# Kernel optimization log

Measured on AMD Instinct MI355X. Metric: run time of the kernel, lower is better.

## Reference

```python
import jax, jax.numpy as jnp
import numpy as np

DIM = 1024
N_HEADS = 16
HEAD_DIM = DIM // N_HEADS


def setup_inputs() -> dict:
    key = jax.random.key(0)
    ks = jax.random.split(key, 5)
    x = jax.random.normal(ks[0], (2, 2048, DIM), dtype=jnp.float32)
    # nn.Linear-style init scale
    s = 1.0 / np.sqrt(DIM)
    W_qkv = jax.random.uniform(ks[1], (DIM, 3 * DIM), jnp.float32, -s, s)
    b_qkv = jax.random.uniform(ks[2], (3 * DIM,), jnp.float32, -s, s)
    W_proj = jax.random.uniform(ks[3], (DIM, DIM), jnp.float32, -s, s)
    b_proj = jax.random.uniform(ks[4], (DIM,), jnp.float32, -s, s)
    return {"x": x, "W_qkv": W_qkv, "b_qkv": b_qkv, "W_proj": W_proj, "b_proj": b_proj}


def reference(x, W_qkv, b_qkv, W_proj, b_proj):
    B, S, D = x.shape
    scale = HEAD_DIM ** -0.5
    qkv = x @ W_qkv + b_qkv                                   # [B,S,3D]
    qkv = qkv.reshape(B, S, 3, N_HEADS, HEAD_DIM)
    q = qkv[:, :, 0].transpose(0, 2, 1, 3)                    # [B,H,S,d]
    k = qkv[:, :, 1].transpose(0, 2, 1, 3)
    v = qkv[:, :, 2].transpose(0, 2, 1, 3)
    attn = jnp.einsum('bhqd,bhkd->bhqk', q, k) * scale        # [B,H,S,S]
    attn = jax.nn.softmax(attn, axis=-1)
    out = jnp.einsum('bhqk,bhkd->bhqd', attn, v)              # [B,H,S,d]
    out = out.transpose(0, 2, 1, 3).reshape(B, S, D)
    return out @ W_proj + b_proj
```

## Files before the change

### kernel.cpp

```cpp
#include <hip/hip_runtime.h>
#include <stdint.h>

typedef unsigned short u16;
typedef __attribute__((ext_vector_type(8))) short bf16x8;
typedef __attribute__((ext_vector_type(4))) float f32x4;
typedef __attribute__((ext_vector_type(16))) float f32x16;
typedef __attribute__((ext_vector_type(4))) u16 us4;
typedef __attribute__((ext_vector_type(8))) u16 us8;

__device__ __forceinline__ u16 f2bf(float f) {
  union { float f; unsigned u; } v; v.f = f;
  unsigned r = v.u + 0x7fffu + ((v.u >> 16) & 1u);
  return (u16)(r >> 16);
}

__device__ __forceinline__ unsigned cvtpk(float a, float b) {
  unsigned r;
  asm("v_cvt_pk_bf16_f32 %0, %1, %2" : "=v"(r) : "v"(a), "v"(b));
  return r;
}

__device__ __forceinline__ float fast_exp2(float x) {
#if __has_builtin(__builtin_amdgcn_exp2f)
  return __builtin_amdgcn_exp2f(x);
#else
  return exp2f(x);
#endif
}

__device__ __forceinline__ void gld16(const void* g, void* l) {
  __builtin_amdgcn_global_load_lds(
      (const __attribute__((address_space(1))) void*)g,
      (__attribute__((address_space(3))) void*)l, 16, 0, 0);
}

__global__ void prep_kernel(const float* __restrict__ x, u16* __restrict__ Xb,
                            const float* __restrict__ Wqkv, u16* __restrict__ Wqkt,
                            const float* __restrict__ Wproj, u16* __restrict__ Wpt) {
  __shared__ u16 tile[64][33];
  const int blk = blockIdx.x;
  if (blk < 4096) {
    const int i = blk * 256 + threadIdx.x;
    f32x4 v = ((const f32x4*)x)[i];
    us4 r;
#pragma unroll
    for (int j = 0; j < 4; ++j) r[j] = f2bf(v[j]);
    ((us4*)Xb)[i] = r;
    return;
  }
  const float* in;
  u16* out;
  int C, t;
  if (blk < 5632) { in = Wqkv; out = Wqkt; C = 3072; t = blk - 4096; }
  else            { in = Wproj; out = Wpt; C = 1024; t = blk - 5632; }
  const int R = 1024;
  const int gx = (C == 3072) ? (t % 96) : (t % 32);
  const int gy = (C == 3072) ? (t / 96) : (t / 32);
  const int tx = threadIdx.x & 31, ty = threadIdx.x >> 5;
  const int c0 = gx * 32, r0 = gy * 64;
#pragma unroll
  for (int j = 0; j < 8; ++j)
    tile[ty + j * 8][tx] = f2bf(in[(size_t)(r0 + ty + j * 8) * C + c0 + tx]);
  __syncthreads();
  const int oc = threadIdx.x >> 3, ob = (threadIdx.x & 7) * 8;
  us8 o;
#pragma unroll
  for (int k = 0; k < 8; ++k) o[k] = tile[ob + k][oc];
  *(us8*)(&out[(size_t)(c0 + oc) * R + r0 + ob]) = o;
}

__global__ __launch_bounds__(256) void qkv_gemm_kernel(
    const u16* __restrict__ A, const u16* __restrict__ Bt, const float* __restrict__ bias,
    u16* __restrict__ Qb, u16* __restrict__ Kb, u16* __restrict__ Vtb) {
  __shared__ u16 sm[17408];
  u16* As = sm;
  u16* Bs = sm + 4096;
  const int tid = threadIdx.x;
  const int w = tid >> 6, l = tid & 63, quad = l >> 4, lanelo = l & 15;
  const int wr = w >> 1, wc = w & 1;
  const int flat = blockIdx.x + 32 * blockIdx.y;
  const int xcd = flat & 7, lid = flat >> 3;
  const long m0 = (long)((xcd >> 1) * 8 + (lid & 7)) * 128;
  const long n0 = (long)((xcd & 1) * 12 + (lid >> 3)) * 128;

  f32x4 acc[4][4];
#pragma unroll
  for (int i = 0; i < 4; ++i)
#pragma unroll
    for (int j = 0; j < 4; ++j) acc[i][j] = (f32x4){0.f, 0.f, 0.f, 0.f};

  const u16* ag = A + (m0 + w * 32 + (l >> 2)) * 1024 + (l & 3) * 8;
  const u16* bg = Bt + (n0 + w * 32 + (l >> 2)) * 1024 + (l & 3) * 8;
  u16* asl = As + w * 1024;
  u16* bsl = Bs + w * 1024;

  for (int kt = 0; kt < 32; ++kt) {
    const int ko = kt * 32;
    gld16(ag + ko, asl);
    gld16(ag + 16 * 1024 + ko, asl + 512);
    gld16(bg + ko, bsl);
    gld16(bg + 16 * 1024 + ko, bsl + 512);
    __syncthreads();
    bf16x8 af[4], bf[4];
#pragma unroll
    for (int mt = 0; mt < 4; ++mt)
      af[mt] = *(const bf16x8*)(As + (wr * 64 + mt * 16 + lanelo) * 32 + quad * 8);
#pragma unroll
    for (int nt = 0; nt < 4; ++nt)
      bf[nt] = *(const bf16x8*)(Bs + (wc * 64 + nt * 16 + lanelo) * 32 + quad * 8);
#pragma unroll
    for (int mt = 0; mt < 4; ++mt)
#pragma unroll
      for (int nt = 0; nt < 4; ++nt)
        acc[mt][nt] = __builtin_amdgcn_mfma_f32_16x16x32_bf16(af[mt], bf[nt], acc[mt][nt], 0, 0, 0);
    __syncthreads();
  }

  const int t = (int)(n0 >> 10);
  const float scl = (t == 0) ? 0.18033688011112042f : 1.0f;

  float bias_v[4];
#pragma unroll
  for (int nt = 0; nt < 4; ++nt) bias_v[nt] = bias[n0 + wc * 64 + nt * 16 + lanelo];

  u16* Ct = sm;
#pragma unroll
  for (int mt = 0; mt < 4; ++mt)
#pragma unroll
    for (int nt = 0; nt < 4; ++nt)
#pragma unroll
      for (int r = 0; r < 4; ++r)
        Ct[(wr * 64 + mt * 16 + quad * 4 + r) * 136 + wc * 64 + nt * 16 + lanelo] =
            f2bf((acc[mt][nt][r] + bias_v[nt]) * scl);
  __syncthreads();

  const int b = (int)(m0 >> 11);
  const int s0 = (int)(m0 & 2047);
  const int h0 = (int)((n0 & 1023) >> 6);

  if (t < 2) {
    u16* dst = (t == 0) ? Qb : Kb;
#pragma unroll
    for (int p = 0; p < 8; ++p) {
      const int hh = p >> 2;
      const int sl = (p & 3) * 32 + (tid >> 3);
      const int c8 = tid & 7;
      us8 v = *(const us8*)(Ct + sl * 136 + hh * 64 + c8 * 8);
      const int pos = (c8 + sl) & 7;
      const size_t off = ((size_t)((b * 16 + h0 + hh) * 2048 + s0 + sl)) * 64 + pos * 8;
      *(us8*)(dst + off) = v;
    }
  } else {
#pragma unroll
    for (int p = 0; p < 8; ++p) {
      const int hh = p >> 2;
      const int dl = (p & 3) * 16 + (tid >> 4);
      const int c16 = tid & 15;
      us8 v;
#pragma unroll
      for (int j = 0; j < 8; ++j) v[j] = Ct[(c16 * 8 + j) * 136 + hh * 64 + dl];
      const int pos = (c16 + dl) & 15;
      const size_t off = ((size_t)((b * 16 + h0 + hh) * 64 + dl)) * 2048 + s0 + pos * 8;
      *(us8*)(Vtb + off) = v;
    }
  }
}

__global__ __launch_bounds__(512, 4) void attn_kernel(
    const u16* __restrict__ Qb, const u16* __restrict__ Kb,
    const u16* __restrict__ Vtb, u16* __restrict__ Ob) {
  __shared__ u16 Ks[2][2][4096];
  __shared__ u16 Vs[2][2][4096];
  const int tid = threadIdx.x;
  const int w8 = tid >> 6;
  const int z = w8 >> 2, w = w8 & 3;
  const int l = tid & 63;
  const int m = l & 31, hi = l >> 5;
  const int fid = blockIdx.x;
  const int head = (fid & 7) + 8 * ((fid >> 3) & 3);
  const int qt = fid >> 5;
  const u16* Qh = Qb + (size_t)head * 2048 * 64;
  const u16* Kh = Kb + (size_t)head * 2048 * 64;
  const u16* Vh = Vtb + (size_t)head * 64 * 2048;

  const int qrow = qt * 128 + w * 32 + m;
  bf16x8 qf[4];
#pragma unroll
  for (int ks = 0; ks < 4; ++ks) {
    const int pos = (ks * 2 + hi + qrow) & 7;
    qf[ks] = *(const bf16x8*)(Qh + (size_t)qrow * 64 + pos * 8);
  }

  bf16x8 onesB;
#pragma unroll
  for (int i = 0; i < 8; ++i) onesB[i] = (short)0x3F80;

  f32x16 o0, o1, sl;
#pragma unroll
  for (int i = 0; i < 16; ++i) { o0[i] = 0.f; o1[i] = 0.f; sl[i] = 0.f; }

  const int i0 = w * 2, i1 = w * 2 + 1;
  const size_t kOff0 = (size_t)i0 * 512 + l * 8;
  const size_t kOff1 = (size_t)i1 * 512 + l * 8;
  const int dd0 = i0 * 8 + (l >> 3), dd1 = i1 * 8 + (l >> 3);
  const int p_ = l & 7;
  const int q0 = (p_ - dd0) & 7, q1 = (p_ - dd1) & 7;
  const size_t vE0 = (size_t)dd0 * 2048 + (size_t)(((q0 + dd0) & 15)) * 8;
  const size_t vO0 = (size_t)dd0 * 2048 + (size_t)(((8 + q0 + dd0) & 15)) * 8;
  const size_t vE1 = (size_t)dd1 * 2048 + (size_t)(((q1 + dd1) & 15)) * 8;
  const size_t vO1 = (size_t)dd1 * 2048 + (size_t)(((8 + q1 + dd1) & 15)) * 8;

  auto stage = [&](int kb, int buf) {
    const u16* kp = Kh + (size_t)kb * 4096;
    gld16(kp + kOff0, &Ks[z][buf][i0 * 512]);
    gld16(kp + kOff1, &Ks[z][buf][i1 * 512]);
    const u16* vp = Vh + (size_t)(kb >> 1) * 128;
    const int odd = kb & 1;
    gld16(vp + (odd ? vO0 : vE0), &Vs[z][buf][i0 * 512]);
    gld16(vp + (odd ? vO1 : vE1), &Vs[z][buf][i1 * 512]);
  };

  int cur = 0;
  stage(z * 16, 0);

  for (int kt = 0; kt < 16; ++kt) {
    __builtin_amdgcn_s_barrier();
    if (kt < 15) {
      stage(z * 16 + kt + 1, cur ^ 1);
      asm volatile("s_waitcnt vmcnt(4)" ::: "memory");
    } else {
      asm volatile("s_waitcnt vmcnt(0)" ::: "memory");
    }
    __builtin_amdgcn_s_barrier();

#pragma unroll
    for (int g = 0; g < 2; ++g) {
      f32x16 st;
#pragma unroll
      for (int i = 0; i < 16; ++i) st[i] = 0.f;
      const int key = g * 32 + m;
      __builtin_amdgcn_s_setprio(1);
#pragma unroll
      for (int ks = 0; ks < 4; ++ks) {
        const int pos = (ks * 2 + hi + key) & 7;
        bf16x8 kf = *(const bf16x8*)(&Ks[z][cur][key * 64 + pos * 8]);
        st = __builtin_amdgcn_mfma_f32_32x32x16_bf16(kf, qf[ks], st, 0, 0, 0);
      }
      __builtin_amdgcn_s_setprio(0);

      float p[16];
#pragma unroll
      for (int r = 0; r < 16; ++r) p[r] = fast_exp2(st[r]);

      unsigned W[8];
#pragma unroll
      for (int i = 0; i < 8; ++i) W[i] = cvtpk(p[2 * i], p[2 * i + 1]);

#pragma unroll
      for (int s = 0; s < 2; ++s) {
        unsigned w0 = W[4 * s], w1 = W[4 * s + 1];
        unsigned w2 = W[4 * s + 2], w3 = W[4 * s + 3];
        asm("v_permlane32_swap_b32 %0, %1" : "+v"(w0), "+v"(w2));
        asm("v_permlane32_swap_b32 %0, %1" : "+v"(w1), "+v"(w3));
        int4 fd;
        fd.x = (int)w0;
        fd.y = (int)w1;
        fd.z = (int)w2;
        fd.w = (int)w3;
        union { int4 i; bf16x8 v; } pu; pu.i = fd;
        const int c = g * 4 + s * 2 + hi;
        __builtin_amdgcn_s_setprio(1);
        sl = __builtin_amdgcn_mfma_f32_32x32x16_bf16(pu.v, onesB, sl, 0, 0, 0);
#pragma unroll
        for (int n = 0; n < 2; ++n) {
          const int d = n * 32 + m;
          const int pos = (c + d) & 7;
          bf16x8 vf = *(const bf16x8*)(&Vs[z][cur][d * 64 + pos * 8]);
          if (n == 0) o0 = __builtin_amdgcn_mfma_f32_32x32x16_bf16(pu.v, vf, o0, 0, 0, 0);
          else        o1 = __builtin_amdgcn_mfma_f32_32x32x16_bf16(pu.v, vf, o1, 0, 0, 0);
        }
        __builtin_amdgcn_s_setprio(0);
      }
    }
    cur ^= 1;
  }
  __syncthreads();

  float* Osl = (float*)Ks;
  float* Lz1 = (float*)Vs;

  if (z == 1) {
    if (m == 0) {
#pragma unroll
      for (int r = 0; r < 16; ++r) {
        const int qlocal = (r & 3) + 8 * (r >> 2) + 4 * hi;
        Lz1[w * 32 + qlocal] = sl[r];
      }
    }
#pragma unroll
    for (int r = 0; r < 16; ++r) {
      const int qlocal = (r & 3) + 8 * (r >> 2) + 4 * hi;
      Osl[w * 2048 + qlocal * 64 + m] = o0[r];
      Osl[w * 2048 + qlocal * 64 + 32 + m] = o1[r];
    }
  }
  __syncthreads();
  if (z == 0) {
    const int b = head >> 4, h = head & 15;
#pragma unroll
    for (int r = 0; r < 16; ++r) {
      const int qlocal = (r & 3) + 8 * (r >> 2) + 4 * hi;
      const float lfull = sl[r] + Lz1[w * 32 + qlocal];
      const float inv = 1.0f / lfull;
      const float v0 = (o0[r] + Osl[w * 2048 + qlocal * 64 + m]) * inv;
      const float v1 = (o1[r] + Osl[w * 2048 + qlocal * 64 + 32 + m]) * inv;
      const size_t base =
          ((size_t)(b * 2048 + qt * 128 + w * 32 + qlocal)) * 1024 + h * 64;
      Ob[base + m] = f2bf(v0);
      Ob[base + 32 + m] = f2bf(v1);
    }
  }
}

__global__ __launch_bounds__(256) void proj_gemm_kernel(
    const u16* __restrict__ A, const u16* __restrict__ Bt,
    const float* __restrict__ bias, float* __restrict__ out) {
  __shared__ u16 sm[6144];
  u16* As = sm;
  u16* Bs = sm + 4096;
  const int tid = threadIdx.x;
  const int w = tid >> 6, l = tid & 63, quad = l >> 4, lanelo = l & 15;
  const int wr = w >> 1, wc = w & 1;
  const int flat = blockIdx.x + 32 * blockIdx.y;
  const int xcd = flat & 7, lid = flat >> 3;
  const long m0 = (long)(xcd * 4 + (lid & 3)) * 128;
  const long n0 = (long)(lid >> 2) * 64;

  f32x4 acc[4][2];
#pragma unroll
  for (int i = 0; i < 4; ++i)
#pragma unroll
    for (int j = 0; j < 2; ++j) acc[i][j] = (f32x4){0.f, 0.f, 0.f, 0.f};

  const u16* ag = A + (m0 + w * 32 + (l >> 2)) * 1024 + (l & 3) * 8;
  const u16* bg = Bt + (n0 + w * 16 + (l >> 2)) * 1024 + (l & 3) * 8;
  u16* asl = As + w * 1024;
  u16* bsl = Bs + w * 512;

  for (int kt = 0; kt < 32; ++kt) {
    const int ko = kt * 32;
    gld16(ag + ko, asl);
    gld16(ag + 16 * 1024 + ko, asl + 512);
    gld16(bg + ko, bsl);
    __syncthreads();
    bf16x8 af[4], bf[2];
#pragma unroll
    for (int mt = 0; mt < 4; ++mt)
      af[mt] = *(const bf16x8*)(As + (wr * 64 + mt * 16 + lanelo) * 32 + quad * 8);
#pragma unroll
    for (int nt = 0; nt < 2; ++nt)
      bf[nt] = *(const bf16x8*)(Bs + (wc * 32 + nt * 16 + lanelo) * 32 + quad * 8);
#pragma unroll
    for (int mt = 0; mt < 4; ++mt)
#pragma unroll
      for (int nt = 0; nt < 2; ++nt)
        acc[mt][nt] = __builtin_amdgcn_mfma_f32_16x16x32_bf16(af[mt], bf[nt], acc[mt][nt], 0, 0, 0);
    __syncthreads();
  }

  float bias_v[2];
#pragma unroll
  for (int nt = 0; nt < 2; ++nt)
    bias_v[nt] = bias[n0 + wc * 32 + nt * 16 + lanelo];

#pragma unroll
  for (int mt = 0; mt < 4; ++mt)
#pragma unroll
    for (int nt = 0; nt < 2; ++nt)
#pragma unroll
      for (int r = 0; r < 4; ++r) {
        const size_t mm = m0 + wr * 64 + mt * 16 + quad * 4 + r;
        const size_t nn = n0 + wc * 32 + nt * 16 + lanelo;
        out[mm * 1024 + nn] = acc[mt][nt][r] + bias_v[nt];
      }
}

extern "C" void kernel_launch(void* const* d_in, const int* in_sizes, int n_in,
                              void* d_out, int out_size, void* d_ws, size_t ws_size,
                              hipStream_t stream) {
  const float* x = (const float*)d_in[0];
  const float* Wqkv = (const float*)d_in[1];
  const float* bqkv = (const float*)d_in[2];
  const float* Wproj = (const float*)d_in[3];
  const float* bproj = (const float*)d_in[4];
  float* out = (float*)d_out;
  char* ws = (char*)d_ws;

  u16* Xb   = (u16*)(ws);
  u16* Ob   = (u16*)(ws);
  u16* Wqkt = (u16*)(ws + 8388608);
  u16* Qb   = (u16*)(ws + 16777216);
  u16* Kb   = (u16*)(ws + 25165824);
  u16* Vtb  = (u16*)(ws + 33554432);
  u16* Wpt  = (u16*)(ws + 41943040);

  prep_kernel<<<6144, 256, 0, stream>>>(x, Xb, Wqkv, Wqkt, Wproj, Wpt);
  qkv_gemm_kernel<<<dim3(32, 24), 256, 0, stream>>>(Xb, Wqkt, bqkv, Qb, Kb, Vtb);
  attn_kernel<<<512, 512, 0, stream>>>(Qb, Kb, Vtb, Ob);
  proj_gemm_kernel<<<dim3(32, 16), 256, 0, stream>>>(Ob, Wpt, bproj, out);
}
```

Before: 183.0 us.

## Process two query tiles per attention block to reuse staged K/V

```diff
diff --git a/kernel.cpp b/kernel.cpp
--- a/kernel.cpp
+++ b/kernel.cpp
@@ -166,7 +166,7 @@
   }
 }
 
-__global__ __launch_bounds__(512, 4) void attn_kernel(
+__global__ __launch_bounds__(512, 2) void attn_kernel(
     const u16* __restrict__ Qb, const u16* __restrict__ Kb,
     const u16* __restrict__ Vtb, u16* __restrict__ Ob) {
   __shared__ u16 Ks[2][2][4096];
@@ -183,21 +183,27 @@
   const u16* Kh = Kb + (size_t)head * 2048 * 64;
   const u16* Vh = Vtb + (size_t)head * 64 * 2048;
 
-  const int qrow = qt * 128 + w * 32 + m;
-  bf16x8 qf[4];
+  const int qrowA = qt * 256 + w * 32 + m;
+  const int qrowB = qrowA + 128;
+  bf16x8 qfA[4], qfB[4];
 #pragma unroll
   for (int ks = 0; ks < 4; ++ks) {
-    const int pos = (ks * 2 + hi + qrow) & 7;
-    qf[ks] = *(const bf16x8*)(Qh + (size_t)qrow * 64 + pos * 8);
+    const int posA = (ks * 2 + hi + qrowA) & 7;
+    qfA[ks] = *(const bf16x8*)(Qh + (size_t)qrowA * 64 + posA * 8);
+    const int posB = (ks * 2 + hi + qrowB) & 7;
+    qfB[ks] = *(const bf16x8*)(Qh + (size_t)qrowB * 64 + posB * 8);
   }
 
   bf16x8 onesB;
 #pragma unroll
   for (int i = 0; i < 8; ++i) onesB[i] = (short)0x3F80;
 
-  f32x16 o0, o1, sl;
-#pragma unroll
-  for (int i = 0; i < 16; ++i) { o0[i] = 0.f; o1[i] = 0.f; sl[i] = 0.f; }
+  f32x16 o0A, o1A, slA, o0B, o1B, slB;
+#pragma unroll
+  for (int i = 0; i < 16; ++i) {
+    o0A[i] = 0.f; o1A[i] = 0.f; slA[i] = 0.f;
+    o0B[i] = 0.f; o1B[i] = 0.f; slB[i] = 0.f;
+  }
 
   const int i0 = w * 2, i1 = w * 2 + 1;
   const size_t kOff0 = (size_t)i0 * 512 + l * 8;
@@ -235,49 +241,63 @@
 
 #pragma unroll
     for (int g = 0; g < 2; ++g) {
-      f32x16 st;
-#pragma unroll
-      for (int i = 0; i < 16; ++i) st[i] = 0.f;
+      f32x16 stA, stB;
+#pragma unroll
+      for (int i = 0; i < 16; ++i) { stA[i] = 0.f; stB[i] = 0.f; }
       const int key = g * 32 + m;
       __builtin_amdgcn_s_setprio(1);
 #pragma unroll
       for (int ks = 0; ks < 4; ++ks) {
         const int pos = (ks * 2 + hi + key) & 7;
         bf16x8 kf = *(const bf16x8*)(&Ks[z][cur][key * 64 + pos * 8]);
-        st = __builtin_amdgcn_mfma_f32_32x32x16_bf16(kf, qf[ks], st, 0, 0, 0);
+        stA = __builtin_amdgcn_mfma_f32_32x32x16_bf16(kf, qfA[ks], stA, 0, 0, 0);
+        stB = __builtin_amdgcn_mfma_f32_32x32x16_bf16(kf, qfB[ks], stB, 0, 0, 0);
       }
       __builtin_amdgcn_s_setprio(0);
 
-      float p[16];
-#pragma unroll
-      for (int r = 0; r < 16; ++r) p[r] = fast_exp2(st[r]);
-
-      unsigned W[8];
-#pragma unroll
-      for (int i = 0; i < 8; ++i) W[i] = cvtpk(p[2 * i], p[2 * i + 1]);
+      float pA[16], pB[16];
+#pragma unroll
+      for (int r = 0; r < 16; ++r) pA[r] = fast_exp2(stA[r]);
+#pragma unroll
+      for (int r = 0; r < 16; ++r) pB[r] = fast_exp2(stB[r]);
+
+      unsigned WA[8], WB[8];
+#pragma unroll
+      for (int i = 0; i < 8; ++i) WA[i] = cvtpk(pA[2 * i], pA[2 * i + 1]);
+#pragma unroll
+      for (int i = 0; i < 8; ++i) WB[i] = cvtpk(pB[2 * i], pB[2 * i + 1]);
 
 #pragma unroll
       for (int s = 0; s < 2; ++s) {
-        unsigned w0 = W[4 * s], w1 = W[4 * s + 1];
-        unsigned w2 = W[4 * s + 2], w3 = W[4 * s + 3];
-        asm("v_permlane32_swap_b32 %0, %1" : "+v"(w0), "+v"(w2));
-        asm("v_permlane32_swap_b32 %0, %1" : "+v"(w1), "+v"(w3));
-        int4 fd;
-        fd.x = (int)w0;
-        fd.y = (int)w1;
-        fd.z = (int)w2;
-        fd.w = (int)w3;
-        union { int4 i; bf16x8 v; } pu; pu.i = fd;
+        unsigned a0 = WA[4 * s], a1 = WA[4 * s + 1];
+        unsigned a2 = WA[4 * s + 2], a3 = WA[4 * s + 3];
+        asm("v_permlane32_swap_b32 %0, %1" : "+v"(a0), "+v"(a2));
+        asm("v_permlane32_swap_b32 %0, %1" : "+v"(a1), "+v"(a3));
+        unsigned b0 = WB[4 * s], b1 = WB[4 * s + 1];
+        unsigned b2 = WB[4 * s + 2], b3 = WB[4 * s + 3];
+        asm("v_permlane32_swap_b32 %0, %1" : "+v"(b0), "+v"(b2));
+        asm("v_permlane32_swap_b32 %0, %1" : "+v"(b1), "+v"(b3));
+        int4 fdA, fdB;
+        fdA.x = (int)a0; fdA.y = (int)a1; fdA.z = (int)a2; fdA.w = (int)a3;
+        fdB.x = (int)b0; fdB.y = (int)b1; fdB.z = (int)b2; fdB.w = (int)b3;
+        union { int4 i; bf16x8 v; } puA, puB;
+        puA.i = fdA; puB.i = fdB;
         const int c = g * 4 + s * 2 + hi;
         __builtin_amdgcn_s_setprio(1);
-        sl = __builtin_amdgcn_mfma_f32_32x32x16_bf16(pu.v, onesB, sl, 0, 0, 0);
+        slA = __builtin_amdgcn_mfma_f32_32x32x16_bf16(puA.v, onesB, slA, 0, 0, 0);
+        slB = __builtin_amdgcn_mfma_f32_32x32x16_bf16(puB.v, onesB, slB, 0, 0, 0);
 #pragma unroll
         for (int n = 0; n < 2; ++n) {
           const int d = n * 32 + m;
           const int pos = (c + d) & 7;
           bf16x8 vf = *(const bf16x8*)(&Vs[z][cur][d * 64 + pos * 8]);
-          if (n == 0) o0 = __builtin_amdgcn_mfma_f32_32x32x16_bf16(pu.v, vf, o0, 0, 0, 0);
-          else        o1 = __builtin_amdgcn_mfma_f32_32x32x16_bf16(pu.v, vf, o1, 0, 0, 0);
+          if (n == 0) {
+            o0A = __builtin_amdgcn_mfma_f32_32x32x16_bf16(puA.v, vf, o0A, 0, 0, 0);
+            o0B = __builtin_amdgcn_mfma_f32_32x32x16_bf16(puB.v, vf, o0B, 0, 0, 0);
+          } else {
+            o1A = __builtin_amdgcn_mfma_f32_32x32x16_bf16(puA.v, vf, o1A, 0, 0, 0);
+            o1B = __builtin_amdgcn_mfma_f32_32x32x16_bf16(puB.v, vf, o1B, 0, 0, 0);
+          }
         }
         __builtin_amdgcn_s_setprio(0);
       }
@@ -288,34 +308,66 @@
 
   float* Osl = (float*)Ks;
   float* Lz1 = (float*)Vs;
+  const int b = head >> 4, h = head & 15;
 
   if (z == 1) {
     if (m == 0) {
 #pragma unroll
       for (int r = 0; r < 16; ++r) {
         const int qlocal = (r & 3) + 8 * (r >> 2) + 4 * hi;
-        Lz1[w * 32 + qlocal] = sl[r];
+        Lz1[w * 32 + qlocal] = slA[r];
       }
     }
 #pragma unroll
     for (int r = 0; r < 16; ++r) {
       const int qlocal = (r & 3) + 8 * (r >> 2) + 4 * hi;
-      Osl[w * 2048 + qlocal * 64 + m] = o0[r];
-      Osl[w * 2048 + qlocal * 64 + 32 + m] = o1[r];
+      Osl[w * 2048 + qlocal * 64 + m] = o0A[r];
+      Osl[w * 2048 + qlocal * 64 + 32 + m] = o1A[r];
     }
   }
   __syncthreads();
   if (z == 0) {
-    const int b = head >> 4, h = head & 15;
 #pragma unroll
     for (int r = 0; r < 16; ++r) {
       const int qlocal = (r & 3) + 8 * (r >> 2) + 4 * hi;
-      const float lfull = sl[r] + Lz1[w * 32 + qlocal];
+      const float lfull = slA[r] + Lz1[w * 32 + qlocal];
       const float inv = 1.0f / lfull;
-      const float v0 = (o0[r] + Osl[w * 2048 + qlocal * 64 + m]) * inv;
-      const float v1 = (o1[r] + Osl[w * 2048 + qlocal * 64 + 32 + m]) * inv;
+      const float v0 = (o0A[r] + Osl[w * 2048 + qlocal * 64 + m]) * inv;
+      const float v1 = (o1A[r] + Osl[w * 2048 + qlocal * 64 + 32 + m]) * inv;
       const size_t base =
-          ((size_t)(b * 2048 + qt * 128 + w * 32 + qlocal)) * 1024 + h * 64;
+          ((size_t)(b * 2048 + qt * 256 + w * 32 + qlocal)) * 1024 + h * 64;
+      Ob[base + m] = f2bf(v0);
+      Ob[base + 32 + m] = f2bf(v1);
+    }
+  }
+  __syncthreads();
+
+  if (z == 1) {
+    if (m == 0) {
+#pragma unroll
+      for (int r = 0; r < 16; ++r) {
+        const int qlocal = (r & 3) + 8 * (r >> 2) + 4 * hi;
+        Lz1[w * 32 + qlocal] = slB[r];
+      }
+    }
+#pragma unroll
+    for (int r = 0; r < 16; ++r) {
+      const int qlocal = (r & 3) + 8 * (r >> 2) + 4 * hi;
+      Osl[w * 2048 + qlocal * 64 + m] = o0B[r];
+      Osl[w * 2048 + qlocal * 64 + 32 + m] = o1B[r];
+    }
+  }
+  __syncthreads();
+  if (z == 0) {
+#pragma unroll
+    for (int r = 0; r < 16; ++r) {
+      const int qlocal = (r & 3) + 8 * (r >> 2) + 4 * hi;
+      const float lfull = slB[r] + Lz1[w * 32 + qlocal];
+      const float inv = 1.0f / lfull;
+      const float v0 = (o0B[r] + Osl[w * 2048 + qlocal * 64 + m]) * inv;
+      const float v1 = (o1B[r] + Osl[w * 2048 + qlocal * 64 + 32 + m]) * inv;
+      const size_t base =
+          ((size_t)(b * 2048 + qt * 256 + 128 + w * 32 + qlocal)) * 1024 + h * 64;
       Ob[base + m] = f2bf(v0);
       Ob[base + 32 + m] = f2bf(v1);
     }
@@ -406,6 +458,6 @@
 
   prep_kernel<<<6144, 256, 0, stream>>>(x, Xb, Wqkv, Wqkt, Wproj, Wpt);
   qkv_gemm_kernel<<<dim3(32, 24), 256, 0, stream>>>(Xb, Wqkt, bqkv, Qb, Kb, Vtb);
-  attn_kernel<<<512, 512, 0, stream>>>(Qb, Kb, Vtb, Ob);
+  attn_kernel<<<256, 512, 0, stream>>>(Qb, Kb, Vtb, Ob);
   proj_gemm_kernel<<<dim3(32, 16), 256, 0, stream>>>(Ob, Wpt, bproj, out);
 }
```

After: 183.8 us. About the same (+0.4%).

## Double-buffer LDS tiles in QKV and projection GEMMs to overlap loads with MFMA

Applied to the files above, without the earlier changes.

```diff
diff --git a/kernel.cpp b/kernel.cpp
--- a/kernel.cpp
+++ b/kernel.cpp
@@ -73,8 +73,6 @@
     const u16* __restrict__ A, const u16* __restrict__ Bt, const float* __restrict__ bias,
     u16* __restrict__ Qb, u16* __restrict__ Kb, u16* __restrict__ Vtb) {
   __shared__ u16 sm[17408];
-  u16* As = sm;
-  u16* Bs = sm + 4096;
   const int tid = threadIdx.x;
   const int w = tid >> 6, l = tid & 63, quad = l >> 4, lanelo = l & 15;
   const int wr = w >> 1, wc = w & 1;
@@ -91,16 +89,32 @@
 
   const u16* ag = A + (m0 + w * 32 + (l >> 2)) * 1024 + (l & 3) * 8;
   const u16* bg = Bt + (n0 + w * 32 + (l >> 2)) * 1024 + (l & 3) * 8;
-  u16* asl = As + w * 1024;
-  u16* bsl = Bs + w * 1024;
+  u16* aw = sm + w * 1024;
+  u16* bw = sm + 8192 + w * 1024;
+
+  auto stage = [&](int kt, int buf) {
+    const int ko = kt * 32;
+    gld16(ag + ko, aw + buf * 4096);
+    gld16(ag + 16 * 1024 + ko, aw + buf * 4096 + 512);
+    gld16(bg + ko, bw + buf * 4096);
+    gld16(bg + 16 * 1024 + ko, bw + buf * 4096 + 512);
+  };
+
+  int cur = 0;
+  stage(0, 0);
 
   for (int kt = 0; kt < 32; ++kt) {
-    const int ko = kt * 32;
-    gld16(ag + ko, asl);
-    gld16(ag + 16 * 1024 + ko, asl + 512);
-    gld16(bg + ko, bsl);
-    gld16(bg + 16 * 1024 + ko, bsl + 512);
-    __syncthreads();
+    __builtin_amdgcn_s_barrier();
+    if (kt < 31) {
+      stage(kt + 1, cur ^ 1);
+      asm volatile("s_waitcnt vmcnt(4)" ::: "memory");
+    } else {
+      asm volatile("s_waitcnt vmcnt(0)" ::: "memory");
+    }
+    __builtin_amdgcn_s_barrier();
+
+    const u16* As = sm + cur * 4096;
+    const u16* Bs = sm + 8192 + cur * 4096;
     bf16x8 af[4], bf[4];
 #pragma unroll
     for (int mt = 0; mt < 4; ++mt)
@@ -113,8 +127,9 @@
 #pragma unroll
       for (int nt = 0; nt < 4; ++nt)
         acc[mt][nt] = __builtin_amdgcn_mfma_f32_16x16x32_bf16(af[mt], bf[nt], acc[mt][nt], 0, 0, 0);
-    __syncthreads();
-  }
+    cur ^= 1;
+  }
+  __syncthreads();
 
   const int t = (int)(n0 >> 10);
   const float scl = (t == 0) ? 0.18033688011112042f : 1.0f;
@@ -325,9 +340,7 @@
 __global__ __launch_bounds__(256) void proj_gemm_kernel(
     const u16* __restrict__ A, const u16* __restrict__ Bt,
     const float* __restrict__ bias, float* __restrict__ out) {
-  __shared__ u16 sm[6144];
-  u16* As = sm;
-  u16* Bs = sm + 4096;
+  __shared__ u16 sm[12288];
   const int tid = threadIdx.x;
   const int w = tid >> 6, l = tid & 63, quad = l >> 4, lanelo = l & 15;
   const int wr = w >> 1, wc = w & 1;
@@ -344,15 +357,31 @@
 
   const u16* ag = A + (m0 + w * 32 + (l >> 2)) * 1024 + (l & 3) * 8;
   const u16* bg = Bt + (n0 + w * 16 + (l >> 2)) * 1024 + (l & 3) * 8;
-  u16* asl = As + w * 1024;
-  u16* bsl = Bs + w * 512;
+  u16* aw = sm + w * 1024;
+  u16* bw = sm + 8192 + w * 512;
+
+  auto stage = [&](int kt, int buf) {
+    const int ko = kt * 32;
+    gld16(ag + ko, aw + buf * 4096);
+    gld16(ag + 16 * 1024 + ko, aw + buf * 4096 + 512);
+    gld16(bg + ko, bw + buf * 2048);
+  };
+
+  int cur = 0;
+  stage(0, 0);
 
   for (int kt = 0; kt < 32; ++kt) {
-    const int ko = kt * 32;
-    gld16(ag + ko, asl);
-    gld16(ag + 16 * 1024 + ko, asl + 512);
-    gld16(bg + ko, bsl);
-    __syncthreads();
+    __builtin_amdgcn_s_barrier();
+    if (kt < 31) {
+      stage(kt + 1, cur ^ 1);
+      asm volatile("s_waitcnt vmcnt(3)" ::: "memory");
+    } else {
+      asm volatile("s_waitcnt vmcnt(0)" ::: "memory");
+    }
+    __builtin_amdgcn_s_barrier();
+
+    const u16* As = sm + cur * 4096;
+    const u16* Bs = sm + 8192 + cur * 2048;
     bf16x8 af[4], bf[2];
 #pragma unroll
     for (int mt = 0; mt < 4; ++mt)
@@ -365,7 +394,7 @@
 #pragma unroll
       for (int nt = 0; nt < 2; ++nt)
         acc[mt][nt] = __builtin_amdgcn_mfma_f32_16x16x32_bf16(af[mt], bf[nt], acc[mt][nt], 0, 0, 0);
-    __syncthreads();
+    cur ^= 1;
   }
 
   float bias_v[2];
```

Measured after the change: 186.7 us. 1.02x slower.

## Double K-step per barrier in GEMMs and shrink transpose tiles in prep

Applied to the files above, without the earlier changes.

```diff
diff --git a/kernel.cpp b/kernel.cpp
--- a/kernel.cpp
+++ b/kernel.cpp
@@ -37,7 +37,7 @@
 __global__ void prep_kernel(const float* __restrict__ x, u16* __restrict__ Xb,
                             const float* __restrict__ Wqkv, u16* __restrict__ Wqkt,
                             const float* __restrict__ Wproj, u16* __restrict__ Wpt) {
-  __shared__ u16 tile[64][33];
+  __shared__ u16 tile[32][33];
   const int blk = blockIdx.x;
   if (blk < 4096) {
     const int i = blk * 256 + threadIdx.x;
@@ -50,31 +50,26 @@
   }
   const float* in;
   u16* out;
-  int C, t;
-  if (blk < 5632) { in = Wqkv; out = Wqkt; C = 3072; t = blk - 4096; }
-  else            { in = Wproj; out = Wpt; C = 1024; t = blk - 5632; }
-  const int R = 1024;
+  int R, C, t;
+  if (blk < 7168) { in = Wqkv; out = Wqkt; R = 1024; C = 3072; t = blk - 4096; }
+  else            { in = Wproj; out = Wpt; R = 1024; C = 1024; t = blk - 7168; }
   const int gx = (C == 3072) ? (t % 96) : (t % 32);
   const int gy = (C == 3072) ? (t / 96) : (t / 32);
   const int tx = threadIdx.x & 31, ty = threadIdx.x >> 5;
-  const int c0 = gx * 32, r0 = gy * 64;
-#pragma unroll
-  for (int j = 0; j < 8; ++j)
+  const int c0 = gx * 32, r0 = gy * 32;
+#pragma unroll
+  for (int j = 0; j < 4; ++j)
     tile[ty + j * 8][tx] = f2bf(in[(size_t)(r0 + ty + j * 8) * C + c0 + tx]);
   __syncthreads();
-  const int oc = threadIdx.x >> 3, ob = (threadIdx.x & 7) * 8;
-  us8 o;
-#pragma unroll
-  for (int k = 0; k < 8; ++k) o[k] = tile[ob + k][oc];
-  *(us8*)(&out[(size_t)(c0 + oc) * R + r0 + ob]) = o;
+#pragma unroll
+  for (int j = 0; j < 4; ++j)
+    out[(size_t)(c0 + ty + j * 8) * R + r0 + tx] = tile[tx][ty + j * 8];
 }
 
 __global__ __launch_bounds__(256) void qkv_gemm_kernel(
     const u16* __restrict__ A, const u16* __restrict__ Bt, const float* __restrict__ bias,
     u16* __restrict__ Qb, u16* __restrict__ Kb, u16* __restrict__ Vtb) {
   __shared__ u16 sm[17408];
-  u16* As = sm;
-  u16* Bs = sm + 4096;
   const int tid = threadIdx.x;
   const int w = tid >> 6, l = tid & 63, quad = l >> 4, lanelo = l & 15;
   const int wr = w >> 1, wc = w & 1;
@@ -91,23 +86,45 @@
 
   const u16* ag = A + (m0 + w * 32 + (l >> 2)) * 1024 + (l & 3) * 8;
   const u16* bg = Bt + (n0 + w * 32 + (l >> 2)) * 1024 + (l & 3) * 8;
-  u16* asl = As + w * 1024;
-  u16* bsl = Bs + w * 1024;
-
-  for (int kt = 0; kt < 32; ++kt) {
-    const int ko = kt * 32;
-    gld16(ag + ko, asl);
-    gld16(ag + 16 * 1024 + ko, asl + 512);
-    gld16(bg + ko, bsl);
-    gld16(bg + 16 * 1024 + ko, bsl + 512);
+  u16* const a0 = sm + w * 1024;
+  u16* const a1 = sm + 4096 + w * 1024;
+  u16* const b0 = sm + 8192 + w * 1024;
+  u16* const b1 = sm + 12288 + w * 1024;
+
+  for (int kt = 0; kt < 16; ++kt) {
+    const int ko = kt * 64;
+    gld16(ag + ko, a0);
+    gld16(ag + 16 * 1024 + ko, a0 + 512);
+    gld16(bg + ko, b0);
+    gld16(bg + 16 * 1024 + ko, b0 + 512);
+    gld16(ag + ko + 32, a1);
+    gld16(ag + 16 * 1024 + ko + 32, a1 + 512);
+    gld16(bg + ko + 32, b1);
+    gld16(bg + 16 * 1024 + ko + 32, b1 + 512);
     __syncthreads();
+
+    const u16* As0 = sm;
+    const u16* As1 = sm + 4096;
+    const u16* Bs0 = sm + 8192;
+    const u16* Bs1 = sm + 12288;
     bf16x8 af[4], bf[4];
 #pragma unroll
     for (int mt = 0; mt < 4; ++mt)
-      af[mt] = *(const bf16x8*)(As + (wr * 64 + mt * 16 + lanelo) * 32 + quad * 8);
+      af[mt] = *(const bf16x8*)(As0 + (wr * 64 + mt * 16 + lanelo) * 32 + quad * 8);
 #pragma unroll
     for (int nt = 0; nt < 4; ++nt)
-      bf[nt] = *(const bf16x8*)(Bs + (wc * 64 + nt * 16 + lanelo) * 32 + quad * 8);
+      bf[nt] = *(const bf16x8*)(Bs0 + (wc * 64 + nt * 16 + lanelo) * 32 + quad * 8);
+#pragma unroll
+    for (int mt = 0; mt < 4; ++mt)
+#pragma unroll
+      for (int nt = 0; nt < 4; ++nt)
+        acc[mt][nt] = __builtin_amdgcn_mfma_f32_16x16x32_bf16(af[mt], bf[nt], acc[mt][nt], 0, 0, 0);
+#pragma unroll
+    for (int mt = 0; mt < 4; ++mt)
+      af[mt] = *(const bf16x8*)(As1 + (wr * 64 + mt * 16 + lanelo) * 32 + quad * 8);
+#pragma unroll
+    for (int nt = 0; nt < 4; ++nt)
+      bf[nt] = *(const bf16x8*)(Bs1 + (wc * 64 + nt * 16 + lanelo) * 32 + quad * 8);
 #pragma unroll
     for (int mt = 0; mt < 4; ++mt)
 #pragma unroll
@@ -325,9 +342,7 @@
 __global__ __launch_bounds__(256) void proj_gemm_kernel(
     const u16* __restrict__ A, const u16* __restrict__ Bt,
     const float* __restrict__ bias, float* __restrict__ out) {
-  __shared__ u16 sm[6144];
-  u16* As = sm;
-  u16* Bs = sm + 4096;
+  __shared__ u16 sm[12288];
   const int tid = threadIdx.x;
   const int w = tid >> 6, l = tid & 63, quad = l >> 4, lanelo = l & 15;
   const int wr = w >> 1, wc = w & 1;
@@ -344,22 +359,43 @@
 
   const u16* ag = A + (m0 + w * 32 + (l >> 2)) * 1024 + (l & 3) * 8;
   const u16* bg = Bt + (n0 + w * 16 + (l >> 2)) * 1024 + (l & 3) * 8;
-  u16* asl = As + w * 1024;
-  u16* bsl = Bs + w * 512;
-
-  for (int kt = 0; kt < 32; ++kt) {
-    const int ko = kt * 32;
-    gld16(ag + ko, asl);
-    gld16(ag + 16 * 1024 + ko, asl + 512);
-    gld16(bg + ko, bsl);
+  u16* const a0 = sm + w * 1024;
+  u16* const a1 = sm + 4096 + w * 1024;
+  u16* const b0 = sm + 8192 + w * 512;
+  u16* const b1 = sm + 10240 + w * 512;
+
+  for (int kt = 0; kt < 16; ++kt) {
+    const int ko = kt * 64;
+    gld16(ag + ko, a0);
+    gld16(ag + 16 * 1024 + ko, a0 + 512);
+    gld16(bg + ko, b0);
+    gld16(ag + ko + 32, a1);
+    gld16(ag + 16 * 1024 + ko + 32, a1 + 512);
+    gld16(bg + ko + 32, b1);
     __syncthreads();
+
+    const u16* As0 = sm;
+    const u16* As1 = sm + 4096;
+    const u16* Bs0 = sm + 8192;
+    const u16* Bs1 = sm + 10240;
     bf16x8 af[4], bf[2];
 #pragma unroll
     for (int mt = 0; mt < 4; ++mt)
-      af[mt] = *(const bf16x8*)(As + (wr * 64 + mt * 16 + lanelo) * 32 + quad * 8);
+      af[mt] = *(const bf16x8*)(As0 + (wr * 64 + mt * 16 + lanelo) * 32 + quad * 8);
 #pragma unroll
     for (int nt = 0; nt < 2; ++nt)
-      bf[nt] = *(const bf16x8*)(Bs + (wc * 32 + nt * 16 + lanelo) * 32 + quad * 8);
+      bf[nt] = *(const bf16x8*)(Bs0 + (wc * 32 + nt * 16 + lanelo) * 32 + quad * 8);
+#pragma unroll
+    for (int mt = 0; mt < 4; ++mt)
+#pragma unroll
+      for (int nt = 0; nt < 2; ++nt)
+        acc[mt][nt] = __builtin_amdgcn_mfma_f32_16x16x32_bf16(af[mt], bf[nt], acc[mt][nt], 0, 0, 0);
+#pragma unroll
+    for (int mt = 0; mt < 4; ++mt)
+      af[mt] = *(const bf16x8*)(As1 + (wr * 64 + mt * 16 + lanelo) * 32 + quad * 8);
+#pragma unroll
+    for (int nt = 0; nt < 2; ++nt)
+      bf[nt] = *(const bf16x8*)(Bs1 + (wc * 32 + nt * 16 + lanelo) * 32 + quad * 8);
 #pragma unroll
     for (int mt = 0; mt < 4; ++mt)
 #pragma unroll
@@ -404,7 +440,7 @@
   u16* Vtb  = (u16*)(ws + 33554432);
   u16* Wpt  = (u16*)(ws + 41943040);
 
-  prep_kernel<<<6144, 256, 0, stream>>>(x, Xb, Wqkv, Wqkt, Wproj, Wpt);
+  prep_kernel<<<8192, 256, 0, stream>>>(x, Xb, Wqkv, Wqkt, Wproj, Wpt);
   qkv_gemm_kernel<<<dim3(32, 24), 256, 0, stream>>>(Xb, Wqkt, bqkv, Qb, Kb, Vtb);
   attn_kernel<<<512, 512, 0, stream>>>(Qb, Kb, Vtb, Ob);
   proj_gemm_kernel<<<dim3(32, 16), 256, 0, stream>>>(Ob, Wpt, bproj, out);
```

After: 188.2 us. 2.8% more time.
